# Optimization experiments

Measured on AMD Instinct MI355X. Metric: run time of the kernel, lower is better.

The kernel has to match this reference:

```python
import jax, jax.numpy as jnp
import numpy as np


def setup_inputs() -> dict:
    key = jax.random.key(0)
    B, S, D = 4, 8192, 768
    x = jax.random.normal(key, (B, S, D), dtype=jnp.float32)
    return {"x": x}


def reference(x) -> jnp.ndarray:
    # FNet mixing: FFT along seq axis, then FFT along hidden axis, take real part.
    # Equivalent to the original nested map_fn(tf.signal.fft) over transposed slices.
    g = jnp.fft.fft2(x.astype(jnp.complex64), axes=(1, 2))  # [B, S, D] complex64
    return jnp.real(g)
```

## Files before the change

kernel.cpp:

```cpp
#include <hip/hip_runtime.h>
#include <math.h>


#define S_LEN 8192
#define D_LEN 768
#define NK2 33
#define ROWS_PB (128 * NK2)
#define TWO_PI 6.28318530717958647692f

__device__ __forceinline__ int dr64(int p) {
    return ((p & 3) << 4) | (((p >> 2) & 3) << 2) | (p >> 4);
}
__device__ __forceinline__ int dr128(int p) {
    return ((p & 1) << 6) | (((p >> 1) & 3) << 4) | (((p >> 3) & 3) << 2) | (p >> 5);
}
__device__ __forceinline__ int dr256(int p) {
    return ((p & 3) << 6) | (((p >> 2) & 3) << 4) | (((p >> 4) & 3) << 2) | (p >> 6);
}
__device__ __forceinline__ int F2(int pos) {
    return 4 * pos + (pos >> 2);
}

#define BFLY4(zre, zim, a0, a1, a2, a3, w1, w2, w3)                            \
    {                                                                          \
        float ar = zre[a0], ai = zim[a0], br = zre[a1], bi = zim[a1];          \
        float cr = zre[a2], ci = zim[a2], er = zre[a3], ei = zim[a3];          \
        float t0r = ar + cr, t0i = ai + ci, t1r = ar - cr, t1i = ai - ci;      \
        float t2r = br + er, t2i = bi + ei, t3r = br - er, t3i = bi - ei;      \
        zre[a0] = t0r + t2r; zim[a0] = t0i + t2i;                              \
        float B1r = t1r + t3i, B1i = t1i - t3r;                                \
        zre[a1] = B1r * w1.x - B1i * w1.y; zim[a1] = B1r * w1.y + B1i * w1.x;  \
        float B2r = t0r - t2r, B2i = t0i - t2i;                                \
        zre[a2] = B2r * w2.x - B2i * w2.y; zim[a2] = B2r * w2.y + B2i * w2.x;  \
        float B3r = t1r - t3i, B3i = t1i + t3r;                                \
        zre[a3] = B3r * w3.x - B3i * w3.y; zim[a3] = B3r * w3.y + B3i * w3.x;  \
    }

__global__ __launch_bounds__(256) void fft_s1_kernel(const float* __restrict__ x,
                                                     float2* __restrict__ Y,
                                                     int b0) {
    __shared__ float zre[64 * 32], zim[64 * 32];
    __shared__ float2 t64[64];
    const int bid = blockIdx.x;
    const int dt = bid % 12;
    const int n1 = (bid / 12) % 128;
    const int bb = bid / (12 * 128);
    const int b = b0 + bb;
    const int t = threadIdx.x;
    const int c = t & 31;
    const int g = t >> 5;

    if (t < 64) {
        float s, co;
        sincosf(-TWO_PI * (float)t / 64.0f, &s, &co);
        t64[t] = make_float2(co, s);
    }

    const size_t xbase = ((size_t)b * S_LEN + n1) * D_LEN + dt * 64 + 2 * c;
    for (int n2 = g; n2 < 64; n2 += 8) {
        const float2 v = *(const float2*)(x + xbase + (size_t)n2 * 128 * D_LEN);
        zre[n2 * 32 + c] = v.x;
        zim[n2 * 32 + c] = v.y;
    }
    __syncthreads();

    #pragma unroll
    for (int it = 0; it < 2; ++it) {
        const int p = g + 8 * it;
        const int a0 = p * 32 + c;
        const float2 w1 = t64[p], w2 = t64[2 * p], w3 = t64[3 * p];
        BFLY4(zre, zim, a0, a0 + 16 * 32, a0 + 32 * 32, a0 + 48 * 32, w1, w2, w3);
    }
    __syncthreads();
    #pragma unroll
    for (int it = 0; it < 2; ++it) {
        const int i = g + 8 * it;
        const int blk = i >> 2, p = i & 3;
        const int base = blk * 16 + p;
        const int a0 = base * 32 + c;
        const float2 w1 = t64[4 * p], w2 = t64[8 * p], w3 = t64[12 * p];
        BFLY4(zre, zim, a0, a0 + 4 * 32, a0 + 8 * 32, a0 + 12 * 32, w1, w2, w3);
    }
    __syncthreads();
    const float2 wid = make_float2(1.0f, 0.0f);
    #pragma unroll
    for (int it = 0; it < 2; ++it) {
        const int i = g + 8 * it;
        const int a0 = (4 * i) * 32 + c;
        BFLY4(zre, zim, a0, a0 + 32, a0 + 2 * 32, a0 + 3 * 32, wid, wid, wid);
    }
    __syncthreads();

    for (int k2 = g; k2 <= 32; k2 += 8) {
        const int p1 = dr64(k2);
        const int p2 = dr64((64 - k2) & 63);
        float zr1 = zre[p1 * 32 + c], zi1 = zim[p1 * 32 + c];
        float zr2 = zre[p2 * 32 + c], zi2 = zim[p2 * 32 + c];
        float Ar = 0.5f * (zr1 + zr2), Ai = 0.5f * (zi1 - zi2);
        float Br = 0.5f * (zi1 + zi2), Bi = -0.5f * (zr1 - zr2);
        const size_t rc = (size_t)bb * ROWS_PB + (size_t)n1 * NK2 + k2;
        const size_t idx = rc * D_LEN + dt * 64 + 2 * c;
        *(float4*)(Y + idx) = make_float4(Ar, Ai, Br, Bi);
    }
}

__global__ __launch_bounds__(256) void fft_s2_kernel(float2* __restrict__ Y) {
    __shared__ float sre[128 * 32], sim[128 * 32];
    __shared__ float2 pt[128];
    __shared__ float2 t128[128];
    const int bid = blockIdx.x;
    const int dt = bid % 24;
    const int k2 = (bid / 24) % NK2;
    const int bb = bid / (24 * NK2);
    const int t = threadIdx.x;
    const int d = t & 31;
    const int g = t >> 5;

    if (t < 128) {
        float s, co;
        sincosf(-TWO_PI * (float)(t * k2) / 8192.0f, &s, &co);
        pt[t] = make_float2(co, s);
        sincosf(-TWO_PI * (float)t / 128.0f, &s, &co);
        t128[t] = make_float2(co, s);
    }
    __syncthreads();

    const size_t base_rc = (size_t)bb * ROWS_PB + k2;
    const int col = dt * 32 + d;
    for (int j = g; j < 128; j += 8) {
        const float2 v = Y[(base_rc + (size_t)j * NK2) * D_LEN + col];
        const float2 w = pt[j];
        sre[j * 32 + d] = v.x * w.x - v.y * w.y;
        sim[j * 32 + d] = v.x * w.y + v.y * w.x;
    }
    __syncthreads();

    #pragma unroll
    for (int it = 0; it < 4; ++it) {
        const int p = g + 8 * it;
        const int a0 = p * 32 + d;
        const float2 w1 = t128[p], w2 = t128[2 * p], w3 = t128[3 * p];
        BFLY4(sre, sim, a0, a0 + 32 * 32, a0 + 64 * 32, a0 + 96 * 32, w1, w2, w3);
    }
    __syncthreads();
    #pragma unroll
    for (int it = 0; it < 4; ++it) {
        const int i = g + 8 * it;
        const int blk = i >> 3, p = i & 7;
        const int a0 = (blk * 32 + p) * 32 + d;
        const float2 w1 = t128[4 * p], w2 = t128[8 * p], w3 = t128[12 * p];
        BFLY4(sre, sim, a0, a0 + 8 * 32, a0 + 16 * 32, a0 + 24 * 32, w1, w2, w3);
    }
    __syncthreads();
    #pragma unroll
    for (int it = 0; it < 4; ++it) {
        const int i = g + 8 * it;
        const int blk = i >> 1, p = i & 1;
        const int a0 = (blk * 8 + p) * 32 + d;
        const float2 w1 = t128[16 * p], w2 = t128[32 * p], w3 = t128[48 * p];
        BFLY4(sre, sim, a0, a0 + 2 * 32, a0 + 4 * 32, a0 + 6 * 32, w1, w2, w3);
    }
    __syncthreads();
    #pragma unroll
    for (int it = 0; it < 8; ++it) {
        const int i = g + 8 * it;
        const int a0 = (2 * i) * 32 + d, a1 = a0 + 32;
        float ar = sre[a0], ai = sim[a0], br = sre[a1], bi = sim[a1];
        sre[a0] = ar + br; sim[a0] = ai + bi;
        sre[a1] = ar - br; sim[a1] = ai - bi;
    }
    __syncthreads();

    for (int j = g; j < 128; j += 8) {
        const int k1 = dr128(j);
        Y[(base_rc + (size_t)k1 * NK2) * D_LEN + col] =
            make_float2(sre[j * 32 + d], sim[j * 32 + d]);
    }
}

__global__ __launch_bounds__(256) void fft_d_kernel(const float2* __restrict__ Y,
                                                    float* __restrict__ out,
                                                    int b0) {
    __shared__ float sre[6528], sim[6528];
    __shared__ float2 t768[256];
    const int t = threadIdx.x;
    const int rc0 = blockIdx.x * 8;

    {
        float s, co;
        sincosf(-TWO_PI * (float)t / 768.0f, &s, &co);
        t768[t] = make_float2(co, s);
    }

    {
        const int rw = t >> 5;
        const int q = t & 31;
        const size_t grow = (size_t)(rc0 + rw) * D_LEN;
        #pragma unroll
        for (int jl = 0; jl < 24; ++jl) {
            const int n = q + 32 * jl;
            const float2 v = Y[grow + n];
            const int pos = (n % 3) * 256 + n / 3;
            const int fi = 8 * pos + 2 * (pos >> 2) + rw;
            sre[fi] = v.x;
            sim[fi] = v.y;
        }
    }
    __syncthreads();

    const int m = t & 3;
    const int q2 = t >> 2;
    float2* s2re = (float2*)sre;
    float2* s2im = (float2*)sim;

#define BFLY4V(a0, a1, a2, a3, w1, w2, w3)                                      \
    {                                                                           \
        float2 ar = s2re[a0], ai = s2im[a0], br = s2re[a1], bi = s2im[a1];      \
        float2 cr = s2re[a2], ci = s2im[a2], er = s2re[a3], ei = s2im[a3];      \
        float2 t0r = make_float2(ar.x + cr.x, ar.y + cr.y);                     \
        float2 t0i = make_float2(ai.x + ci.x, ai.y + ci.y);                     \
        float2 t1r = make_float2(ar.x - cr.x, ar.y - cr.y);                     \
        float2 t1i = make_float2(ai.x - ci.x, ai.y - ci.y);                     \
        float2 t2r = make_float2(br.x + er.x, br.y + er.y);                     \
        float2 t2i = make_float2(bi.x + ei.x, bi.y + ei.y);                     \
        float2 t3r = make_float2(br.x - er.x, br.y - er.y);                     \
        float2 t3i = make_float2(bi.x - ei.x, bi.y - ei.y);                     \
        s2re[a0] = make_float2(t0r.x + t2r.x, t0r.y + t2r.y);                   \
        s2im[a0] = make_float2(t0i.x + t2i.x, t0i.y + t2i.y);                   \
        float2 B1r = make_float2(t1r.x + t3i.x, t1r.y + t3i.y);                 \
        float2 B1i = make_float2(t1i.x - t3r.x, t1i.y - t3r.y);                 \
        s2re[a1] = make_float2(B1r.x * w1.x - B1i.x * w1.y,                     \
                               B1r.y * w1.x - B1i.y * w1.y);                    \
        s2im[a1] = make_float2(B1r.x * w1.y + B1i.x * w1.x,                     \
                               B1r.y * w1.y + B1i.y * w1.x);                    \
        float2 B2r = make_float2(t0r.x - t2r.x, t0r.y - t2r.y);                 \
        float2 B2i = make_float2(t0i.x - t2i.x, t0i.y - t2i.y);                 \
        s2re[a2] = make_float2(B2r.x * w2.x - B2i.x * w2.y,                     \
                               B2r.y * w2.x - B2i.y * w2.y);                    \
        s2im[a2] = make_float2(B2r.x * w2.y + B2i.x * w2.x,                     \
                               B2r.y * w2.y + B2i.y * w2.x);                    \
        float2 B3r = make_float2(t1r.x - t3i.x, t1r.y - t3i.y);                 \
        float2 B3i = make_float2(t1i.x + t3r.x, t1i.y + t3r.y);                 \
        s2re[a3] = make_float2(B3r.x * w3.x - B3i.x * w3.y,                     \
                               B3r.y * w3.x - B3i.y * w3.y);                    \
        s2im[a3] = make_float2(B3r.x * w3.y + B3i.x * w3.x,                     \
                               B3r.y * w3.y + B3i.y * w3.x);                    \
    }
#define CSQ(w) make_float2((w).x * (w).x - (w).y * (w).y, 2.0f * (w).x * (w).y)
#define CMU(a, b) make_float2((a).x * (b).x - (a).y * (b).y,                    \
                              (a).x * (b).y + (a).y * (b).x)

    #pragma unroll
    for (int jj = 0; jj < 3; ++jj) {
        const int bf = q2 + 64 * jj;
        const int sub = bf >> 6;
        const int p = bf & 63;
        const int base = sub * 256 + p;
        const float2 w1 = t768[3 * p];
        const float2 w2 = CSQ(w1);
        const float2 w3 = CMU(w1, w2);
        BFLY4V(F2(base) + m, F2(base + 64) + m, F2(base + 128) + m,
               F2(base + 192) + m, w1, w2, w3);
    }
    __syncthreads();
    #pragma unroll
    for (int jj = 0; jj < 3; ++jj) {
        const int bf = q2 + 64 * jj;
        const int sub = bf >> 6;
        const int i = bf & 63;
        const int blk = i >> 4, p = i & 15;
        const int base = sub * 256 + blk * 64 + p;
        const float2 w1 = t768[12 * p];
        const float2 w2 = CSQ(w1);
        const float2 w3 = CMU(w1, w2);
        BFLY4V(F2(base) + m, F2(base + 16) + m, F2(base + 32) + m,
               F2(base + 48) + m, w1, w2, w3);
    }
    __syncthreads();
    #pragma unroll
    for (int jj = 0; jj < 3; ++jj) {
        const int bf = q2 + 64 * jj;
        const int sub = bf >> 6;
        const int i = bf & 63;
        const int blk = i >> 2, p = i & 3;
        const int base = sub * 256 + blk * 16 + p;
        const float2 w1 = t768[48 * p];
        const float2 w2 = CSQ(w1);
        const float2 w3 = CMU(w1, w2);
        BFLY4V(F2(base) + m, F2(base + 4) + m, F2(base + 8) + m,
               F2(base + 12) + m, w1, w2, w3);
    }
    __syncthreads();
    {
        const float2 wid = make_float2(1.0f, 0.0f);
        #pragma unroll
        for (int jj = 0; jj < 3; ++jj) {
            const int bf = q2 + 64 * jj;
            const int sub = bf >> 6;
            const int i = bf & 63;
            const int base = sub * 256 + 4 * i;
            BFLY4V(F2(base) + m, F2(base + 1) + m, F2(base + 2) + m,
                   F2(base + 3) + m, wid, wid, wid);
        }
    }
    __syncthreads();

    size_t obase[8], mbase[8];
    bool domir[8];
    #pragma unroll
    for (int rr = 0; rr < 8; ++rr) {
        const int rc = rc0 + rr;
        const int bb = rc / ROWS_PB;
        const int qq = rc - bb * ROWS_PB;
        const int K1 = qq / NK2;
        const int K2 = qq - K1 * NK2;
        const int srow = 64 * K1 + K2;
        const size_t bs = (size_t)(b0 + bb) * S_LEN;
        obase[rr] = (bs + srow) * D_LEN;
        mbase[rr] = (bs + (S_LEN - srow)) * D_LEN;
        domir[rr] = (K2 >= 1 && K2 <= 31);
    }

    const float W3r = -0.5f, W3i = -0.86602540378443864676f;
    const int kk = t;
    const int j8 = dr256(kk);
    const int e0 = F2(j8), e1 = F2(256 + j8), e2 = F2(512 + j8);
    const float2 w = t768[kk];
    const float c1 = w.x, s1 = w.y;
    const float c2 = c1 * c1 - s1 * s1, s2_ = 2.0f * c1 * s1;
    const int md0 = (kk == 0) ? 0 : (768 - kk);
    #pragma unroll
    for (int i2 = 0; i2 < 4; ++i2) {
        const float2 u0r = s2re[e0 + i2], u0i = s2im[e0 + i2];
        const float2 u1r = s2re[e1 + i2], u1i = s2im[e1 + i2];
        const float2 u2r = s2re[e2 + i2], u2i = s2im[e2 + i2];
        const float2 v1r = make_float2(u1r.x * c1 - u1i.x * s1, u1r.y * c1 - u1i.y * s1);
        const float2 v1i = make_float2(u1r.x * s1 + u1i.x * c1, u1r.y * s1 + u1i.y * c1);
        const float2 v2r = make_float2(u2r.x * c2 - u2i.x * s2_, u2r.y * c2 - u2i.y * s2_);
        const float2 v2i = make_float2(u2r.x * s2_ + u2i.x * c2, u2r.y * s2_ + u2i.y * c2);
        const float2 y0 = make_float2(u0r.x + v1r.x + v2r.x, u0r.y + v1r.y + v2r.y);
        const float2 y1 = make_float2(
            u0r.x + (v1r.x * W3r - v1i.x * W3i) + (v2r.x * W3r + v2i.x * W3i),
            u0r.y + (v1r.y * W3r - v1i.y * W3i) + (v2r.y * W3r + v2i.y * W3i));
        const float2 y2 = make_float2(
            u0r.x + (v1r.x * W3r + v1i.x * W3i) + (v2r.x * W3r - v2i.x * W3i),
            u0r.y + (v1r.y * W3r + v1i.y * W3i) + (v2r.y * W3r - v2i.y * W3i));
        #pragma unroll
        for (int h = 0; h < 2; ++h) {
            const int rr = 2 * i2 + h;
            const float v0 = h ? y0.y : y0.x;
            const float v1 = h ? y1.y : y1.x;
            const float v2 = h ? y2.y : y2.x;
            out[obase[rr] + kk] = v0;
            out[obase[rr] + 256 + kk] = v1;
            out[obase[rr] + 512 + kk] = v2;
            if (domir[rr]) {
                out[mbase[rr] + md0] = v0;
                out[mbase[rr] + 512 - kk] = v1;
                out[mbase[rr] + 256 - kk] = v2;
            }
        }
    }
#undef BFLY4V
#undef CSQ
#undef CMU
}

extern "C" void kernel_launch(void* const* d_in, const int* in_sizes, int n_in,
                              void* d_out, int out_size, void* d_ws, size_t ws_size,
                              hipStream_t stream) {
    const float* x = (const float*)d_in[0];
    float* out = (float*)d_out;
    float2* Y = (float2*)d_ws;

    const size_t full_plane_bytes = (size_t)4 * ROWS_PB * D_LEN * sizeof(float2);
    const size_t half_plane_bytes = full_plane_bytes / 2;
    int nb;
    if (ws_size >= full_plane_bytes) nb = 4;
    else if (ws_size >= half_plane_bytes) nb = 2;
    else return;

    for (int b0 = 0; b0 < 4; b0 += nb) {
        fft_s1_kernel<<<dim3(nb * 128 * 12), dim3(256), 0, stream>>>(x, Y, b0);
        fft_s2_kernel<<<dim3(nb * NK2 * 24), dim3(256), 0, stream>>>(Y);
        fft_d_kernel<<<dim3(nb * ROWS_PB / 8), dim3(256), 0, stream>>>(Y, out, b0);
    }
}
```

Measured before the change: 126.1 us.

## Rewrite stage-1 64-point FFT as register radix-8 x8 decomposition

The first-stage 64-point FFT kernel now loads eight strided samples per thread into registers and does an in-register radix-8 FFT. It then applies twiddles and exchanges once through padded shared memory (stride 33) for a second radix-8 pass. This replaces three shared-memory radix-4 passes with a bit-reversal gather, cutting barriers and LDS traffic. The cost is higher register pressure, and twiddles are now built by repeated multiplication instead of a precomputed table, which may add small rounding error.

Result: faster. 122.8 us (-2.6%).

```diff
diff --git a/kernel.cpp b/kernel.cpp
--- a/kernel.cpp
+++ b/kernel.cpp
@@ -8,9 +8,6 @@
 #define ROWS_PB (128 * NK2)
 #define TWO_PI 6.28318530717958647692f
 
-__device__ __forceinline__ int dr64(int p) {
-    return ((p & 3) << 4) | (((p >> 2) & 3) << 2) | (p >> 4);
-}
 __device__ __forceinline__ int dr128(int p) {
     return ((p & 1) << 6) | (((p >> 1) & 3) << 4) | (((p >> 3) & 3) << 2) | (p >> 5);
 }
@@ -19,6 +16,38 @@
 }
 __device__ __forceinline__ int F2(int pos) {
     return 4 * pos + (pos >> 2);
+}
+
+__device__ __forceinline__ float2 cadd(float2 a, float2 b) {
+    return make_float2(a.x + b.x, a.y + b.y);
+}
+__device__ __forceinline__ float2 csub(float2 a, float2 b) {
+    return make_float2(a.x - b.x, a.y - b.y);
+}
+__device__ __forceinline__ float2 cmulf(float2 a, float2 b) {
+    return make_float2(a.x * b.x - a.y * b.y, a.x * b.y + a.y * b.x);
+}
+__device__ __forceinline__ float2 mul_mi(float2 a) {
+    return make_float2(a.y, -a.x);
+}
+
+__device__ __forceinline__ void fft8(const float2* a, float2* X) {
+    const float R2 = 0.70710678118654752440f;
+    float2 u0 = cadd(a[0], a[4]), v0 = csub(a[0], a[4]);
+    float2 u1 = cadd(a[1], a[5]), v1 = csub(a[1], a[5]);
+    float2 u2 = cadd(a[2], a[6]), v2 = csub(a[2], a[6]);
+    float2 u3 = cadd(a[3], a[7]), v3 = csub(a[3], a[7]);
+    v1 = make_float2(R2 * (v1.x + v1.y), R2 * (v1.y - v1.x));
+    v2 = mul_mi(v2);
+    v3 = make_float2(R2 * (v3.y - v3.x), -R2 * (v3.x + v3.y));
+    float2 e0 = cadd(u0, u2), o0 = csub(u0, u2);
+    float2 e1 = cadd(u1, u3), o1 = mul_mi(csub(u1, u3));
+    X[0] = cadd(e0, e1); X[4] = csub(e0, e1);
+    X[2] = cadd(o0, o1); X[6] = csub(o0, o1);
+    float2 f0 = cadd(v0, v2), p0 = csub(v0, v2);
+    float2 f1 = cadd(v1, v3), p1 = mul_mi(csub(v1, v3));
+    X[1] = cadd(f0, f1); X[5] = csub(f0, f1);
+    X[3] = cadd(p0, p1); X[7] = csub(p0, p1);
 }
 
 #define BFLY4(zre, zim, a0, a1, a2, a3, w1, w2, w3)                            \
@@ -39,8 +68,7 @@
 __global__ __launch_bounds__(256) void fft_s1_kernel(const float* __restrict__ x,
                                                      float2* __restrict__ Y,
                                                      int b0) {
-    __shared__ float zre[64 * 32], zim[64 * 32];
-    __shared__ float2 t64[64];
+    __shared__ float2 Z[64 * 33];
     const int bid = blockIdx.x;
     const int dt = bid % 12;
     const int n1 = (bid / 12) % 128;
@@ -48,59 +76,55 @@
     const int b = b0 + bb;
     const int t = threadIdx.x;
     const int c = t & 31;
-    const int g = t >> 5;
-
-    if (t < 64) {
+    const int na = t >> 5;
+
+    float2 v[8];
+    const size_t xbase = ((size_t)b * S_LEN + n1 + 128 * na) * D_LEN + dt * 64 + 2 * c;
+    #pragma unroll
+    for (int nb2 = 0; nb2 < 8; ++nb2) {
+        v[nb2] = *(const float2*)(x + xbase + (size_t)nb2 * 1024 * D_LEN);
+    }
+
+    float2 g[8];
+    fft8(v, g);
+
+    {
         float s, co;
-        sincosf(-TWO_PI * (float)t / 64.0f, &s, &co);
-        t64[t] = make_float2(co, s);
-    }
-
-    const size_t xbase = ((size_t)b * S_LEN + n1) * D_LEN + dt * 64 + 2 * c;
-    for (int n2 = g; n2 < 64; n2 += 8) {
-        const float2 v = *(const float2*)(x + xbase + (size_t)n2 * 128 * D_LEN);
-        zre[n2 * 32 + c] = v.x;
-        zim[n2 * 32 + c] = v.y;
-    }
-    __syncthreads();
-
-    #pragma unroll
-    for (int it = 0; it < 2; ++it) {
-        const int p = g + 8 * it;
-        const int a0 = p * 32 + c;
-        const float2 w1 = t64[p], w2 = t64[2 * p], w3 = t64[3 * p];
-        BFLY4(zre, zim, a0, a0 + 16 * 32, a0 + 32 * 32, a0 + 48 * 32, w1, w2, w3);
-    }
-    __syncthreads();
-    #pragma unroll
-    for (int it = 0; it < 2; ++it) {
-        const int i = g + 8 * it;
-        const int blk = i >> 2, p = i & 3;
-        const int base = blk * 16 + p;
-        const int a0 = base * 32 + c;
-        const float2 w1 = t64[4 * p], w2 = t64[8 * p], w3 = t64[12 * p];
-        BFLY4(zre, zim, a0, a0 + 4 * 32, a0 + 8 * 32, a0 + 12 * 32, w1, w2, w3);
-    }
-    __syncthreads();
-    const float2 wid = make_float2(1.0f, 0.0f);
-    #pragma unroll
-    for (int it = 0; it < 2; ++it) {
-        const int i = g + 8 * it;
-        const int a0 = (4 * i) * 32 + c;
-        BFLY4(zre, zim, a0, a0 + 32, a0 + 2 * 32, a0 + 3 * 32, wid, wid, wid);
-    }
-    __syncthreads();
-
-    for (int k2 = g; k2 <= 32; k2 += 8) {
-        const int p1 = dr64(k2);
-        const int p2 = dr64((64 - k2) & 63);
-        float zr1 = zre[p1 * 32 + c], zi1 = zim[p1 * 32 + c];
-        float zr2 = zre[p2 * 32 + c], zi2 = zim[p2 * 32 + c];
-        float Ar = 0.5f * (zr1 + zr2), Ai = 0.5f * (zi1 - zi2);
-        float Br = 0.5f * (zi1 + zi2), Bi = -0.5f * (zr1 - zr2);
-        const size_t rc = (size_t)bb * ROWS_PB + (size_t)n1 * NK2 + k2;
-        const size_t idx = rc * D_LEN + dt * 64 + 2 * c;
-        *(float4*)(Y + idx) = make_float4(Ar, Ai, Br, Bi);
+        sincosf(-TWO_PI * (float)na / 64.0f, &s, &co);
+        const float2 w = make_float2(co, s);
+        float2 wk = w;
+        #pragma unroll
+        for (int k = 1; k < 8; ++k) {
+            g[k] = cmulf(g[k], wk);
+            wk = cmulf(wk, w);
+        }
+    }
+
+    #pragma unroll
+    for (int k = 0; k < 8; ++k) Z[(8 * k + na) * 33 + c] = g[k];
+    __syncthreads();
+
+    float2 h[8], r[8];
+    #pragma unroll
+    for (int j = 0; j < 8; ++j) h[j] = Z[(8 * na + j) * 33 + c];
+    fft8(h, r);
+    __syncthreads();
+    #pragma unroll
+    for (int ka = 0; ka < 8; ++ka) Z[(na + 8 * ka) * 33 + c] = r[ka];
+    __syncthreads();
+
+    const size_t rcb = (size_t)bb * ROWS_PB + (size_t)n1 * NK2;
+    #pragma unroll
+    for (int it = 0; it < 5; ++it) {
+        const int k2 = na + 8 * it;
+        if (k2 <= 32) {
+            const float2 z1 = Z[k2 * 33 + c];
+            const float2 z2 = Z[((64 - k2) & 63) * 33 + c];
+            const float Ar = 0.5f * (z1.x + z2.x), Ai = 0.5f * (z1.y - z2.y);
+            const float Br = 0.5f * (z1.y + z2.y), Bi = -0.5f * (z1.x - z2.x);
+            const size_t idx = (rcb + k2) * D_LEN + dt * 64 + 2 * c;
+            *(float4*)(Y + idx) = make_float4(Ar, Ai, Br, Bi);
+        }
     }
 }
 
```
